# Kernel tuning notes

Hardware: AMD Instinct MI355X
Metric: run time of the kernel (lower is better)

The kernel has to match this reference:

```python
import jax, jax.numpy as jnp
import numpy as np

N, D, K = 131072, 128, 256
MAX_ITER = 8
TOL = 1e-4


def setup_inputs() -> dict:
    key = jax.random.key(0)
    kx, kp = jax.random.split(key)
    X = jax.random.normal(kx, (N, D), dtype=jnp.float32)
    # torch.randperm(N)[:K] -> distinct initial centroid indices
    init_idx = jax.random.permutation(kp, N)[:K]
    return {"X": X, "init_idx": init_idx, "max_iter": MAX_ITER}


def _assign(X, centroids):
    # argmin over Euclidean distance == argmin over squared distance;
    # ||x||^2 is constant per row so drop it: d2[n,k] = ||c_k||^2 - 2 x_n . c_k
    d2 = jnp.sum(centroids * centroids, axis=1)[None, :] - 2.0 * (X @ centroids.T)  # [N,K]
    return jnp.argmin(d2, axis=1)  # [N]


def reference(X, init_idx, max_iter):
    n = X.shape[0]
    centroids0 = X[init_idx]  # [K,D]

    def step(carry, _):
        centroids, done = carry
        labels = _assign(X, centroids)  # [N]
        sums = jax.ops.segment_sum(X, labels, num_segments=K)  # [K,D]
        counts = jax.ops.segment_sum(jnp.ones((n,), X.dtype), labels, num_segments=K)  # [K]
        new_c = sums / counts[:, None]  # empty cluster -> 0/0 = nan (matches torch mean of empty)
        shift = jnp.linalg.norm(new_c - centroids)
        new_done = jnp.logical_or(done, shift < TOL)
        # torch breaks BEFORE assigning new centroids when converged
        centroids = jnp.where(new_done, centroids, new_c)
        return (centroids, new_done), labels

    (centroids, _), labels_hist = jax.lax.scan(
        step, (centroids0, jnp.array(False)), None, length=max_iter
    )
    labels = labels_hist[-1]
    return labels, centroids
```

## Files before the change

### kernel.cpp

```cpp
#include <hip/hip_runtime.h>

#define NP 131072
#define DD 128
#define KK 256
#define MAXIT 8
#define TOLSQ (1e-4f * 1e-4f)
#define POSB 256
#define UPIPE 8

typedef _Float16 half8 __attribute__((ext_vector_type(8)));
typedef float f32x4 __attribute__((ext_vector_type(4)));

struct Ws {
    float C[KK * DD];
    float newC[KK * DD];
    float cnorm[KK];
    float sums[KK * DD];
    float shiftsq;
    int done;
    int ilab[NP];
    int counts[KK];
    int cursor[KK];
    int ordlab[NP];
    alignas(16) _Float16 Csh[KK * DD];
    alignas(16) _Float16 Csl[KK * DD];
    alignas(16) _Float16 Xsh[(size_t)NP * DD];
    alignas(16) _Float16 Xsl[(size_t)NP * DD];
};

__global__ void k_init(const float* __restrict__ X, const int* __restrict__ idx,
                       float* __restrict__ C, int* __restrict__ done) {
    int k = blockIdx.x, d = threadIdx.x;
    C[k * DD + d] = X[(size_t)idx[k] * DD + d];
    if (k == 0 && d == 0) *done = 0;
}

__global__ void k_split(const float* __restrict__ X, _Float16* __restrict__ Xh,
                        _Float16* __restrict__ Xl) {
    size_t idx = (size_t)blockIdx.x * 256 + threadIdx.x;
    int lane = idx & 63;
    size_t g16k = idx >> 6;
    size_t point = (g16k >> 2) * 16 + (lane & 15);
    int dim0 = (int)(g16k & 3) * 32 + (lane >> 4) * 8;
    const f32x4* s4 = (const f32x4*)(X + point * DD + dim0);
    f32x4 a = s4[0], b = s4[1];
    half8 h, l;
#pragma unroll
    for (int j = 0; j < 4; j++) {
        _Float16 hi = (_Float16)a[j];
        h[j] = hi; l[j] = (_Float16)(a[j] - (float)hi);
    }
#pragma unroll
    for (int j = 0; j < 4; j++) {
        _Float16 hi = (_Float16)b[j];
        h[4 + j] = hi; l[4 + j] = (_Float16)(b[j] - (float)hi);
    }
    *(half8*)(Xh + idx * 8) = h;
    *(half8*)(Xl + idx * 8) = l;
}

__global__ void k_prep0(const float* __restrict__ C, float* __restrict__ cnorm,
                        _Float16* __restrict__ Ch, _Float16* __restrict__ Cl,
                        int* __restrict__ counts, int* __restrict__ cursor) {
    int k = blockIdx.x, d = threadIdx.x;
    float v = C[k * DD + d];
    _Float16 hi = (_Float16)v;
    int ct = k >> 4, l4 = k & 15, ks = d >> 5, q = (d >> 3) & 3, j = d & 7;
    size_t dst = ((size_t)(ks * 16 + ct) * 64 + (q * 16 + l4)) * 8 + j;
    Ch[dst] = hi;
    Cl[dst] = (_Float16)(v - (float)hi);
    __shared__ float red[DD];
    red[d] = v * v;
    __syncthreads();
    for (int s = DD / 2; s > 0; s >>= 1) {
        if (d < s) red[d] += red[d + s];
        __syncthreads();
    }
    if (d == 0) {
        cnorm[k] = red[0];
        counts[k] = 0;
        cursor[k] = 0;
    }
}

__global__ __launch_bounds__(512, 2) void k_assign(
    const _Float16* __restrict__ Xh, const _Float16* __restrict__ Xl,
    const _Float16* __restrict__ Ch, const _Float16* __restrict__ Cl,
    const float* __restrict__ cnorm, float* __restrict__ outlab,
    int* __restrict__ ilab, int* __restrict__ counts,
    float* __restrict__ shiftsq) {
    __shared__ unsigned long long mbuf[4][512];
    __shared__ int hist[KK];
    const int tid = threadIdx.x;
    const int wave = tid >> 6;
    const int lane = tid & 63;
    const int l4 = lane & 15, g = lane >> 4;
    const int pgrp = wave >> 2;
    const int q = wave & 3;

    if (blockIdx.x == 0 && tid == 0) *shiftsq = 0.0f;
    if (tid < KK) hist[tid] = 0;

    half8 Bh[4][4], Bl[4][4];
#pragma unroll
    for (int ks = 0; ks < 4; ks++)
#pragma unroll
        for (int c = 0; c < 4; c++) {
            size_t off = ((size_t)(ks * 16 + q * 4 + c) * 64 + lane) * 8;
            Bh[ks][c] = *(const half8*)(Ch + off);
            Bl[ks][c] = *(const half8*)(Cl + off);
        }

    float cn[4];
#pragma unroll
    for (int c = 0; c < 4; c++) cn[c] = cnorm[(q * 4 + c) * 16 + l4];

    const int gb = blockIdx.x * 32 + pgrp * 2;
    size_t a0 = ((size_t)(gb * 4) * 64 + lane) * 8;
    size_t a1 = ((size_t)((gb + 1) * 4) * 64 + lane) * 8;
    half8 ah0 = *(const half8*)(Xh + a0), al0 = *(const half8*)(Xl + a0);
    half8 ah1 = *(const half8*)(Xh + a1), al1 = *(const half8*)(Xl + a1);

#pragma unroll 1
    for (int r = 0; r < 8; r++) {
        f32x4 acc[2][4];
#pragma unroll
        for (int pg = 0; pg < 2; pg++)
#pragma unroll
            for (int c = 0; c < 4; c++) acc[pg][c] = (f32x4){0.f, 0.f, 0.f, 0.f};

#pragma unroll
        for (int ks = 0; ks < 4; ks++) {
            int ns = r * 4 + ks + 1;
            ns = ns > 31 ? 31 : ns;
            const int ng16 = blockIdx.x * 32 + (ns >> 2) * 4 + pgrp * 2;
            const int nks = ns & 3;
            const size_t b0 = ((size_t)(ng16 * 4 + nks) * 64 + lane) * 8;
            const size_t b1 = ((size_t)((ng16 + 1) * 4 + nks) * 64 + lane) * 8;
            half8 nh0 = *(const half8*)(Xh + b0), nl0 = *(const half8*)(Xl + b0);
            half8 nh1 = *(const half8*)(Xh + b1), nl1 = *(const half8*)(Xl + b1);

#pragma unroll
            for (int c = 0; c < 4; c++) {
                acc[0][c] = __builtin_amdgcn_mfma_f32_16x16x32_f16(al0, Bh[ks][c], acc[0][c], 0, 0, 0);
                acc[1][c] = __builtin_amdgcn_mfma_f32_16x16x32_f16(al1, Bh[ks][c], acc[1][c], 0, 0, 0);
            }
#pragma unroll
            for (int c = 0; c < 4; c++) {
                acc[0][c] = __builtin_amdgcn_mfma_f32_16x16x32_f16(ah0, Bl[ks][c], acc[0][c], 0, 0, 0);
                acc[1][c] = __builtin_amdgcn_mfma_f32_16x16x32_f16(ah1, Bl[ks][c], acc[1][c], 0, 0, 0);
            }
#pragma unroll
            for (int c = 0; c < 4; c++) {
                acc[0][c] = __builtin_amdgcn_mfma_f32_16x16x32_f16(ah0, Bh[ks][c], acc[0][c], 0, 0, 0);
                acc[1][c] = __builtin_amdgcn_mfma_f32_16x16x32_f16(ah1, Bh[ks][c], acc[1][c], 0, 0, 0);
            }
            ah0 = nh0; al0 = nl0; ah1 = nh1; al1 = nl1;
        }

        unsigned long long best[2][4];
#pragma unroll
        for (int pg = 0; pg < 2; pg++)
#pragma unroll
            for (int rr = 0; rr < 4; rr++) best[pg][rr] = ~0ull;

#pragma unroll
        for (int pg = 0; pg < 2; pg++)
#pragma unroll
            for (int c = 0; c < 4; c++)
#pragma unroll
                for (int rr = 0; rr < 4; rr++) {
                    float s = fmaf(-2.0f, acc[pg][c][rr], cn[c]);
                    if (__builtin_isnan(s)) s = -__builtin_inff();
                    unsigned u = __float_as_uint(s);
                    unsigned m = (u >> 31) ? ~u : (u ^ 0x80000000u);
                    unsigned long long key =
                        ((unsigned long long)m << 32) |
                        (unsigned)((q * 4 + c) * 16 + l4);
                    if (key < best[pg][rr]) best[pg][rr] = key;
                }

#pragma unroll
        for (int d = 1; d < 16; d <<= 1)
#pragma unroll
            for (int pg = 0; pg < 2; pg++)
#pragma unroll
                for (int rr = 0; rr < 4; rr++) {
                    unsigned long long o = __shfl_xor(best[pg][rr], d, 64);
                    if (o < best[pg][rr]) best[pg][rr] = o;
                }

        if (l4 == 0) {
#pragma unroll
            for (int pg = 0; pg < 2; pg++)
#pragma unroll
                for (int rr = 0; rr < 4; rr++) {
                    int pl = (r * 4 + pgrp * 2 + pg) * 16 + g * 4 + rr;
                    mbuf[q][pl] = best[pg][rr];
                }
        }
    }

    __syncthreads();
    {
        unsigned long long k0 = mbuf[0][tid], k1 = mbuf[1][tid];
        unsigned long long k2 = mbuf[2][tid], k3 = mbuf[3][tid];
        unsigned long long ka = k0 < k1 ? k0 : k1;
        unsigned long long kb = k2 < k3 ? k2 : k3;
        unsigned long long k = ka < kb ? ka : kb;
        int point = blockIdx.x * 512 + tid;
        int lbl = (int)(k & 0x1ff);
        outlab[point] = (float)lbl;
        ilab[point] = lbl;
        atomicAdd(&hist[lbl], 1);
    }
    __syncthreads();
    if (tid < KK) {
        int h = hist[tid];
        if (h) atomicAdd(&counts[tid], h);
    }
}

__global__ __launch_bounds__(256) void k_scatter(
    const int* __restrict__ ilab, const int* __restrict__ counts,
    int* __restrict__ cursor, int* __restrict__ ordlab,
    float* __restrict__ sums) {
    const int t = threadIdx.x;
    const int b = blockIdx.x;

    if (t < 128) sums[b * 128 + t] = 0.0f;

    __shared__ int hist[KK];
    __shared__ int pre[KK];
    __shared__ int gbase[KK];
    hist[t] = 0;
    int c = counts[t];
    pre[t] = c;
    __syncthreads();

    const int p0 = b * 512;
    const int la = ilab[p0 + t];
    const int lb = ilab[p0 + 256 + t];
    atomicAdd(&hist[la], 1);
    atomicAdd(&hist[lb], 1);

#pragma unroll
    for (int d = 1; d < KK; d <<= 1) {
        int v = (t >= d) ? pre[t - d] : 0;
        __syncthreads();
        pre[t] += v;
        __syncthreads();
    }
    int h = hist[t];
    int gb = (pre[t] - c) + (h ? atomicAdd(&cursor[t], h) : 0);
    gbase[t] = gb;
    __syncthreads();
    hist[t] = 0;
    __syncthreads();

    int ra = atomicAdd(&hist[la], 1);
    ordlab[gbase[la] + ra] = (p0 + t) | (la << 17);
    int rb = atomicAdd(&hist[lb], 1);
    ordlab[gbase[lb] + rb] = (p0 + 256 + t) | (lb << 17);
}

__global__ __launch_bounds__(256) void k_sum(
    const float* __restrict__ X, const int* __restrict__ ordlab,
    float* __restrict__ sums) {
    const int t = threadIdx.x;
    const int d = t & 127, h = t >> 7;

    __shared__ int sol[POSB];
    sol[t] = ordlab[blockIdx.x * POSB + t];
    __syncthreads();

    const int PP = POSB / 2;
    float xv[UPIPE], xn[UPIPE];
#pragma unroll
    for (int u = 0; u < UPIPE; u++)
        xv[u] = X[(size_t)(sol[2 * u + h] & 0x1ffff) * DD + d];

    float acc = 0.0f;
    int cur = sol[h] >> 17;

    for (int jb = 0; jb < PP; jb += UPIPE) {
#pragma unroll
        for (int u = 0; u < UPIPE; u++) {
            int nj = jb + u + UPIPE;
            int o = sol[2 * (nj < PP ? nj : PP - 1) + h];
            xn[u] = X[(size_t)(o & 0x1ffff) * DD + d];
        }
#pragma unroll
        for (int u = 0; u < UPIPE; u++) {
            int l = sol[2 * (jb + u) + h] >> 17;
            if (l != cur) {
                atomicAdd(&sums[cur * DD + d], acc);
                acc = 0.0f;
                cur = l;
            }
            acc += xv[u];
        }
#pragma unroll
        for (int u = 0; u < UPIPE; u++) xv[u] = xn[u];
    }
    atomicAdd(&sums[cur * DD + d], acc);
}

__global__ void k_reduce(const float* __restrict__ sums, const int* __restrict__ counts,
                         const float* __restrict__ C, float* __restrict__ newC,
                         float* __restrict__ shiftsq) {
    const int g = blockIdx.x * 256 + threadIdx.x;
    const int k = g >> 7;
    const int t = threadIdx.x;

    float nc = sums[g] / (float)counts[k];
    newC[g] = nc;
    float diff = nc - C[g];

    __shared__ float red[256];
    red[t] = diff * diff;
    __syncthreads();
    for (int st = 128; st > 0; st >>= 1) {
        if (t < st) red[t] += red[t + st];
        __syncthreads();
    }
    if (t == 0) atomicAdd(shiftsq, red[0]);
}

__global__ void k_upprep(const float* __restrict__ newC, float* __restrict__ C,
                         const float* __restrict__ shiftsq, int* __restrict__ done,
                         float* __restrict__ cnorm, _Float16* __restrict__ Ch,
                         _Float16* __restrict__ Cl, int* __restrict__ counts,
                         int* __restrict__ cursor) {
    const int t = threadIdx.x;
    const int k = blockIdx.x * 2 + (t >> 7);
    const int d = t & 127;
    float ss = *shiftsq;
    int nd = (*done != 0) || (ss < TOLSQ);
    float v = nd ? C[k * DD + d] : newC[k * DD + d];
    C[k * DD + d] = v;
    if (blockIdx.x == 0 && t == 0 && nd) *done = 1;
    if (d == 0) {
        counts[k] = 0;
        cursor[k] = 0;
    }

    _Float16 hi = (_Float16)v;
    int ct = k >> 4, l4 = k & 15, ks = d >> 5, q = (d >> 3) & 3, j = d & 7;
    size_t dst = ((size_t)(ks * 16 + ct) * 64 + (q * 16 + l4)) * 8 + j;
    Ch[dst] = hi;
    Cl[dst] = (_Float16)(v - (float)hi);

    __shared__ float red[256];
    red[t] = v * v;
    __syncthreads();
    for (int s = 64; s > 0; s >>= 1) {
        if ((t & 127) < s) red[t] += red[t + s];
        __syncthreads();
    }
    if (d == 0) cnorm[k] = red[t];
}

__global__ void k_final(const float* __restrict__ C, float* __restrict__ out) {
    int i = blockIdx.x * 256 + threadIdx.x;
    out[i] = C[i];
}

extern "C" void kernel_launch(void* const* d_in, const int* in_sizes, int n_in,
                              void* d_out, int out_size, void* d_ws, size_t ws_size,
                              hipStream_t stream) {
    const float* X = (const float*)d_in[0];
    const int* idx = (const int*)d_in[1];
    float* out = (float*)d_out;
    Ws* w = (Ws*)d_ws;

    k_init<<<KK, DD, 0, stream>>>(X, idx, w->C, &w->done);
    k_split<<<(int)((size_t)NP * DD / 8 / 256), 256, 0, stream>>>(X, w->Xsh, w->Xsl);
    k_prep0<<<KK, DD, 0, stream>>>(w->C, w->cnorm, w->Csh, w->Csl, w->counts, w->cursor);

    for (int it = 0; it < MAXIT; it++) {
        k_assign<<<NP / 512, 512, 0, stream>>>(w->Xsh, w->Xsl, w->Csh, w->Csl,
                                               w->cnorm, out, w->ilab, w->counts,
                                               &w->shiftsq);
        k_scatter<<<NP / 512, 256, 0, stream>>>(w->ilab, w->counts, w->cursor,
                                                w->ordlab, w->sums);
        k_sum<<<NP / POSB, 256, 0, stream>>>(X, w->ordlab, w->sums);
        k_reduce<<<KK * DD / 256, 256, 0, stream>>>(w->sums, w->counts, w->C,
                                                    w->newC, &w->shiftsq);
        k_upprep<<<KK / 2, 256, 0, stream>>>(w->newC, w->C, &w->shiftsq, &w->done,
                                             w->cnorm, w->Csh, w->Csl, w->counts,
                                             w->cursor);
    }

    k_final<<<KK * DD / 256, 256, 0, stream>>>(w->C, out + NP);
}
```

Baseline: 631.8 us.

## Replace sort-based segment sum with per-block LDS partial sums and reduction

Drops the counting-sort scatter kernel and the segmented sum over sorted points. Each block of 512 points now accumulates into a full K×D float array in shared memory using LDS atomics. It then writes that array out as one per-block partial, and k_reduce sums the 256 partials per element. This removes the scatter pass, its global cursor atomics and the gather-style reads of X. In exchange it uses about 128KB of LDS per block, which limits occupancy, and moves about 32MB of partials out and back in every iteration.

```diff
diff --git a/kernel.cpp b/kernel.cpp
--- a/kernel.cpp
+++ b/kernel.cpp
@@ -5,7 +5,7 @@
 #define KK 256
 #define MAXIT 8
 #define TOLSQ (1e-4f * 1e-4f)
-#define POSB 256
+#define SB 512
 #define UPIPE 8
 
 typedef _Float16 half8 __attribute__((ext_vector_type(8)));
@@ -15,13 +15,11 @@
     float C[KK * DD];
     float newC[KK * DD];
     float cnorm[KK];
-    float sums[KK * DD];
     float shiftsq;
     int done;
     int ilab[NP];
     int counts[KK];
-    int cursor[KK];
-    int ordlab[NP];
+    alignas(16) float partial[256 * KK * DD];
     alignas(16) _Float16 Csh[KK * DD];
     alignas(16) _Float16 Csl[KK * DD];
     alignas(16) _Float16 Xsh[(size_t)NP * DD];
@@ -61,7 +59,7 @@
 
 __global__ void k_prep0(const float* __restrict__ C, float* __restrict__ cnorm,
                         _Float16* __restrict__ Ch, _Float16* __restrict__ Cl,
-                        int* __restrict__ counts, int* __restrict__ cursor) {
+                        int* __restrict__ counts) {
     int k = blockIdx.x, d = threadIdx.x;
     float v = C[k * DD + d];
     _Float16 hi = (_Float16)v;
@@ -79,7 +77,6 @@
     if (d == 0) {
         cnorm[k] = red[0];
         counts[k] = 0;
-        cursor[k] = 0;
     }
 }
 
@@ -221,103 +218,76 @@
     }
 }
 
-__global__ __launch_bounds__(256) void k_scatter(
-    const int* __restrict__ ilab, const int* __restrict__ counts,
-    int* __restrict__ cursor, int* __restrict__ ordlab,
-    float* __restrict__ sums) {
-    const int t = threadIdx.x;
-    const int b = blockIdx.x;
-
-    if (t < 128) sums[b * 128 + t] = 0.0f;
-
-    __shared__ int hist[KK];
-    __shared__ int pre[KK];
-    __shared__ int gbase[KK];
-    hist[t] = 0;
-    int c = counts[t];
-    pre[t] = c;
-    __syncthreads();
-
-    const int p0 = b * 512;
-    const int la = ilab[p0 + t];
-    const int lb = ilab[p0 + 256 + t];
-    atomicAdd(&hist[la], 1);
-    atomicAdd(&hist[lb], 1);
-
-#pragma unroll
-    for (int d = 1; d < KK; d <<= 1) {
-        int v = (t >= d) ? pre[t - d] : 0;
-        __syncthreads();
-        pre[t] += v;
-        __syncthreads();
-    }
-    int h = hist[t];
-    int gb = (pre[t] - c) + (h ? atomicAdd(&cursor[t], h) : 0);
-    gbase[t] = gb;
-    __syncthreads();
-    hist[t] = 0;
-    __syncthreads();
-
-    int ra = atomicAdd(&hist[la], 1);
-    ordlab[gbase[la] + ra] = (p0 + t) | (la << 17);
-    int rb = atomicAdd(&hist[lb], 1);
-    ordlab[gbase[lb] + rb] = (p0 + 256 + t) | (lb << 17);
-}
-
-__global__ __launch_bounds__(256) void k_sum(
-    const float* __restrict__ X, const int* __restrict__ ordlab,
-    float* __restrict__ sums) {
+__global__ __launch_bounds__(256) void k_sumfuse(
+    const float* __restrict__ X, const int* __restrict__ ilab,
+    float* __restrict__ partial) {
+    __shared__ float ls[KK * DD];
+    __shared__ int sol[SB];
     const int t = threadIdx.x;
     const int d = t & 127, h = t >> 7;
 
-    __shared__ int sol[POSB];
-    sol[t] = ordlab[blockIdx.x * POSB + t];
-    __syncthreads();
-
-    const int PP = POSB / 2;
+    f32x4* lz = (f32x4*)ls;
+#pragma unroll
+    for (int i = 0; i < KK * DD / 4 / 256; i++)
+        lz[t + 256 * i] = (f32x4){0.f, 0.f, 0.f, 0.f};
+    sol[t] = ilab[blockIdx.x * SB + t];
+    sol[t + 256] = ilab[blockIdx.x * SB + 256 + t];
+    __syncthreads();
+
+    const size_t p0 = (size_t)blockIdx.x * SB;
+    const int PP = SB / 2;
     float xv[UPIPE], xn[UPIPE];
-#pragma unroll
-    for (int u = 0; u < UPIPE; u++)
-        xv[u] = X[(size_t)(sol[2 * u + h] & 0x1ffff) * DD + d];
-
-    float acc = 0.0f;
-    int cur = sol[h] >> 17;
-
+    int lv[UPIPE], ln[UPIPE];
+#pragma unroll
+    for (int u = 0; u < UPIPE; u++) {
+        xv[u] = X[(p0 + 2 * u + h) * DD + d];
+        lv[u] = sol[2 * u + h];
+    }
     for (int jb = 0; jb < PP; jb += UPIPE) {
 #pragma unroll
         for (int u = 0; u < UPIPE; u++) {
             int nj = jb + u + UPIPE;
-            int o = sol[2 * (nj < PP ? nj : PP - 1) + h];
-            xn[u] = X[(size_t)(o & 0x1ffff) * DD + d];
+            nj = nj < PP ? nj : PP - 1;
+            xn[u] = X[(p0 + 2 * nj + h) * DD + d];
+            ln[u] = sol[2 * nj + h];
         }
 #pragma unroll
-        for (int u = 0; u < UPIPE; u++) {
-            int l = sol[2 * (jb + u) + h] >> 17;
-            if (l != cur) {
-                atomicAdd(&sums[cur * DD + d], acc);
-                acc = 0.0f;
-                cur = l;
-            }
-            acc += xv[u];
-        }
-#pragma unroll
-        for (int u = 0; u < UPIPE; u++) xv[u] = xn[u];
-    }
-    atomicAdd(&sums[cur * DD + d], acc);
-}
-
-__global__ void k_reduce(const float* __restrict__ sums, const int* __restrict__ counts,
-                         const float* __restrict__ C, float* __restrict__ newC,
-                         float* __restrict__ shiftsq) {
-    const int g = blockIdx.x * 256 + threadIdx.x;
-    const int k = g >> 7;
+        for (int u = 0; u < UPIPE; u++)
+            atomicAdd(&ls[lv[u] * DD + d], xv[u]);
+#pragma unroll
+        for (int u = 0; u < UPIPE; u++) { xv[u] = xn[u]; lv[u] = ln[u]; }
+    }
+    __syncthreads();
+
+    f32x4* gp = (f32x4*)(partial + (size_t)blockIdx.x * KK * DD);
+#pragma unroll
+    for (int i = 0; i < KK * DD / 4 / 256; i++)
+        gp[t + 256 * i] = lz[t + 256 * i];
+}
+
+__global__ __launch_bounds__(256) void k_reduce(
+    const float* __restrict__ partial, const int* __restrict__ counts,
+    const float* __restrict__ C, float* __restrict__ newC,
+    float* __restrict__ shiftsq) {
     const int t = threadIdx.x;
-
-    float nc = sums[g] / (float)counts[k];
-    newC[g] = nc;
-    float diff = nc - C[g];
+    const int g = blockIdx.x * 128 + (t & 127);
+    const int rh = t >> 7;
+    float s = 0.f;
+#pragma unroll 8
+    for (int r = rh * 128; r < rh * 128 + 128; r++)
+        s += partial[(size_t)r * (KK * DD) + g];
 
     __shared__ float red[256];
+    red[t] = s;
+    __syncthreads();
+    float diff = 0.f;
+    if (t < 128) {
+        int k = g >> 7;
+        float nc = (red[t] + red[t + 128]) / (float)counts[k];
+        newC[g] = nc;
+        diff = nc - C[g];
+    }
+    __syncthreads();
     red[t] = diff * diff;
     __syncthreads();
     for (int st = 128; st > 0; st >>= 1) {
@@ -330,8 +300,7 @@
 __global__ void k_upprep(const float* __restrict__ newC, float* __restrict__ C,
                          const float* __restrict__ shiftsq, int* __restrict__ done,
                          float* __restrict__ cnorm, _Float16* __restrict__ Ch,
-                         _Float16* __restrict__ Cl, int* __restrict__ counts,
-                         int* __restrict__ cursor) {
+                         _Float16* __restrict__ Cl, int* __restrict__ counts) {
     const int t = threadIdx.x;
     const int k = blockIdx.x * 2 + (t >> 7);
     const int d = t & 127;
@@ -340,10 +309,7 @@
     float v = nd ? C[k * DD + d] : newC[k * DD + d];
     C[k * DD + d] = v;
     if (blockIdx.x == 0 && t == 0 && nd) *done = 1;
-    if (d == 0) {
-        counts[k] = 0;
-        cursor[k] = 0;
-    }
+    if (d == 0) counts[k] = 0;
 
     _Float16 hi = (_Float16)v;
     int ct = k >> 4, l4 = k & 15, ks = d >> 5, q = (d >> 3) & 3, j = d & 7;
@@ -376,20 +342,17 @@
 
     k_init<<<KK, DD, 0, stream>>>(X, idx, w->C, &w->done);
     k_split<<<(int)((size_t)NP * DD / 8 / 256), 256, 0, stream>>>(X, w->Xsh, w->Xsl);
-    k_prep0<<<KK, DD, 0, stream>>>(w->C, w->cnorm, w->Csh, w->Csl, w->counts, w->cursor);
+    k_prep0<<<KK, DD, 0, stream>>>(w->C, w->cnorm, w->Csh, w->Csl, w->counts);
 
     for (int it = 0; it < MAXIT; it++) {
         k_assign<<<NP / 512, 512, 0, stream>>>(w->Xsh, w->Xsl, w->Csh, w->Csl,
                                                w->cnorm, out, w->ilab, w->counts,
                                                &w->shiftsq);
-        k_scatter<<<NP / 512, 256, 0, stream>>>(w->ilab, w->counts, w->cursor,
-                                                w->ordlab, w->sums);
-        k_sum<<<NP / POSB, 256, 0, stream>>>(X, w->ordlab, w->sums);
-        k_reduce<<<KK * DD / 256, 256, 0, stream>>>(w->sums, w->counts, w->C,
+        k_sumfuse<<<NP / SB, 256, 0, stream>>>(X, w->ilab, w->partial);
+        k_reduce<<<KK * DD / 128, 256, 0, stream>>>(w->partial, w->counts, w->C,
                                                     w->newC, &w->shiftsq);
         k_upprep<<<KK / 2, 256, 0, stream>>>(w->newC, w->C, &w->shiftsq, &w->done,
-                                             w->cnorm, w->Csh, w->Csl, w->counts,
-                                             w->cursor);
+                                             w->cnorm, w->Csh, w->Csl, w->counts);
     }
 
     k_final<<<KK * DD / 256, 256, 0, stream>>>(w->C, out + NP);
```

After: 1.278 ms. 102% more time.
